# Optimization experiments

Measured on AMD Instinct MI355X. Metric: run time of the kernel, lower is better.

## Reference

```python
import jax, jax.numpy as jnp
import numpy as np

EPS = 1e-5

def _bn(t, gamma, beta):
    # training-mode BatchNorm2d: stats over (B,H,W), biased variance
    mean = jnp.mean(t, axis=(0, 2, 3), keepdims=True)
    var = jnp.var(t, axis=(0, 2, 3), keepdims=True)
    tn = (t - mean) * jax.lax.rsqrt(var + EPS)
    return tn * gamma[None, :, None, None] + beta[None, :, None, None]

def setup_inputs() -> dict:
    key = jax.random.key(0)
    ks = jax.random.split(key, 8)
    B, C, H, W = 16, 256, 64, 64
    u, k, v = 4, 16, 256
    s = 1.0 / np.sqrt(C)
    x = jax.random.normal(ks[0], (B, C, H, W), dtype=jnp.float32)
    Wq = jax.random.normal(ks[1], (k, C), dtype=jnp.float32) * s
    bq = jax.random.normal(ks[2], (k,), dtype=jnp.float32) * 0.01
    Wk = jax.random.normal(ks[3], (u * k, C), dtype=jnp.float32) * s
    bk = jax.random.normal(ks[4], (u * k,), dtype=jnp.float32) * 0.01
    Wv = jax.random.normal(ks[5], (u * v, C), dtype=jnp.float32) * s
    bv = jax.random.normal(ks[6], (u * v,), dtype=jnp.float32) * 0.01
    gamma_q = jnp.ones((k,), dtype=jnp.float32)
    beta_q = jnp.zeros((k,), dtype=jnp.float32)
    gamma_v = jnp.ones((u * v,), dtype=jnp.float32)
    beta_v = jnp.zeros((u * v,), dtype=jnp.float32)
    return {"x": x, "Wq": Wq, "bq": bq, "Wk": Wk, "bk": bk, "Wv": Wv, "bv": bv,
            "gamma_q": gamma_q, "beta_q": beta_q, "gamma_v": gamma_v, "beta_v": beta_v}

def reference(x, Wq, bq, Wk, bk, Wv, bv, gamma_q, beta_q, gamma_v, beta_v):
    B, C, H, W = x.shape
    k = Wq.shape[0]
    u = 4
    v = Wv.shape[0] // u
    # 1x1 convs as channel contractions
    Q = jnp.einsum('oc,bchw->bohw', Wq, x) + bq[None, :, None, None]   # [B,k,H,W]
    K = jnp.einsum('oc,bchw->bohw', Wk, x) + bk[None, :, None, None]   # [B,u*k,H,W]
    V = jnp.einsum('oc,bchw->bohw', Wv, x) + bv[None, :, None, None]   # [B,u*v,H,W]
    Q = _bn(Q, gamma_q, beta_q)
    V = _bn(V, gamma_v, beta_v)
    m = H * W
    Q = Q.reshape(B, k, m)          # [B,k,m]
    K = K.reshape(B, u, k, m)       # [B,u,k,m]
    V = V.reshape(B, u, v, m)       # [B,u,v,m]
    K = jax.nn.softmax(K, axis=3)
    context = jnp.einsum('bukm,buvm->bkv', K, V)   # [B,k,v]
    y = jnp.einsum('bkn,bkv->bvn', Q, context)     # [B,v,m]
    return y.reshape(B, v, H, W)
```

## Files before the change

### kernel.cpp

```cpp
#include <hip/hip_runtime.h>
#include <hip/hip_bf16.h>

typedef short s16x8 __attribute__((ext_vector_type(8)));
typedef short s16x4 __attribute__((ext_vector_type(4)));
typedef float f32x4 __attribute__((ext_vector_type(4)));
typedef unsigned u32;
typedef u32 u32x2 __attribute__((ext_vector_type(2)));

#define DI __device__ __forceinline__

constexpr int BB = 16;
constexpr int CC = 256;
constexpr int MM = 4096;
constexpr int KD = 16;
constexpr int UK = 64;
constexpr float EPSV = 1e-5f;

DI unsigned short f2bf(float f) {
  union { float f; unsigned u; } v; v.f = f;
  unsigned r = v.u + 0x7FFFu + ((v.u >> 16) & 1u);
  return (unsigned short)(r >> 16);
}
DI float bfu(unsigned short u) { union { u32 u; float f; } w; w.u = (u32)u << 16; return w.f; }
DI float bflo(u32 v) { union { u32 u; float f; } w; w.u = v << 16; return w.f; }
DI float bfhi(u32 v) { union { u32 u; float f; } w; w.u = v & 0xFFFF0000u; return w.f; }

__global__ __launch_bounds__(256) void k_cvt(const float* __restrict__ x,
    unsigned short* __restrict__ xbf, float* __restrict__ xsump) {
  int bid = blockIdx.x;
  size_t base = (size_t)bid * MM;
  int t = threadIdx.x;
  float s = 0.f;
#pragma unroll
  for (int i = 0; i < 4; ++i) {
    size_t idx = base + (size_t)(i * 256 + t) * 4;
    float4 v = *(const float4*)(x + idx);
    s16x4 c;
    c[0] = (short)f2bf(v.x); c[1] = (short)f2bf(v.y);
    c[2] = (short)f2bf(v.z); c[3] = (short)f2bf(v.w);
    *(s16x4*)&xbf[idx] = c;
    s += v.x + v.y + v.z + v.w;
  }
#pragma unroll
  for (int o = 32; o; o >>= 1) s += __shfl_down(s, o);
  __shared__ float red[4];
  if ((t & 63) == 0) red[t >> 6] = s;
  __syncthreads();
  if (t == 0) xsump[bid] = red[0] + red[1] + red[2] + red[3];
}

__global__ __launch_bounds__(512) void k_gxx(const unsigned short* __restrict__ xbf,
                                             u32* __restrict__ part) {
  int b = blockIdx.x >> 4, mc = blockIdx.x & 15;
  int m0 = mc * 256;
  __shared__ short lds[2][256 * 72];
  int t = threadIdx.x, w = t >> 6, l = t & 63;
  int wr = w >> 2, wc = w & 3;
  int lrow = l & 15, lk8 = (l >> 4) * 8;
  int srow = t >> 3, sseg = (t & 7) * 8;

  const unsigned short* gsrc = xbf + ((size_t)(b * CC + srow)) * MM + m0 + sseg;

  s16x8 rg[4];
#pragma unroll
  for (int i = 0; i < 4; ++i)
    rg[i] = *(const s16x8*)(gsrc + (size_t)i * 64 * MM);
#pragma unroll
  for (int i = 0; i < 4; ++i)
    *(s16x8*)&lds[0][(srow + i * 64) * 72 + sseg] = rg[i];

  f32x4 acc[8][4];
#pragma unroll
  for (int i = 0; i < 8; ++i)
#pragma unroll
    for (int j = 0; j < 4; ++j) acc[i][j] = (f32x4)0.f;

#pragma unroll
  for (int ks = 0; ks < 4; ++ks) {
    __syncthreads();
    if (ks < 3) {
#pragma unroll
      for (int i = 0; i < 4; ++i)
        rg[i] = *(const s16x8*)(gsrc + (size_t)i * 64 * MM + (ks + 1) * 64);
    }
    int buf = ks & 1;
#pragma unroll
    for (int half = 0; half < 2; ++half) {
      s16x8 af[8], bf[4];
#pragma unroll
      for (int i = 0; i < 8; ++i)
        af[i] = *(const s16x8*)&lds[buf][(wr * 128 + i * 16 + lrow) * 72 + half * 32 + lk8];
#pragma unroll
      for (int j = 0; j < 4; ++j)
        bf[j] = *(const s16x8*)&lds[buf][(wc * 64 + j * 16 + lrow) * 72 + half * 32 + lk8];
#pragma unroll
      for (int i = 0; i < 8; ++i)
#pragma unroll
        for (int j = 0; j < 4; ++j)
          acc[i][j] = __builtin_amdgcn_mfma_f32_16x16x32_bf16(af[i], bf[j], acc[i][j], 0, 0, 0);
    }
    if (ks < 3) {
#pragma unroll
      for (int i = 0; i < 4; ++i)
        *(s16x8*)&lds[buf ^ 1][(srow + i * 64) * 72 + sseg] = rg[i];
    }
  }

  size_t pb = (size_t)blockIdx.x * 32768;
#pragma unroll
  for (int i = 0; i < 8; ++i)
#pragma unroll
    for (int j = 0; j < 4; ++j) {
      int tau = (w * 8 + i) * 4 + j;
      u32x2 pk;
      pk[0] = (u32)f2bf(acc[i][j][0]) | ((u32)f2bf(acc[i][j][1]) << 16);
      pk[1] = (u32)f2bf(acc[i][j][2]) | ((u32)f2bf(acc[i][j][3]) << 16);
      *(u32x2*)&part[pb + tau * 128 + l * 2] = pk;
    }
}

__global__ __launch_bounds__(256) void k_gred(const u32* __restrict__ part,
                                              float* __restrict__ G) {
  int q = blockIdx.x * 256 + threadIdx.x;
  float s0 = 0.f, s1 = 0.f;
#pragma unroll 8
  for (int p = 0; p < 256; ++p) {
    u32 v = part[(size_t)p * 32768 + q];
    s0 += bflo(v);
    s1 += bfhi(v);
  }
  int r2 = q & 1, l = (q >> 1) & 63, tau = q >> 7;
  int j = tau & 3, i = (tau >> 2) & 7, w = tau >> 5;
  int wr = w >> 2, wc = w & 3;
  int row = wr * 128 + i * 16 + (l >> 4) * 4 + r2 * 2;
  int col = wc * 64 + j * 16 + (l & 15);
  G[row * 256 + col] = s0;
  G[(row + 1) * 256 + col] = s1;
}

__global__ __launch_bounds__(256) void k_proj(const unsigned short* __restrict__ xbf,
    const float* __restrict__ Wq, const float* __restrict__ bq,
    const float* __restrict__ Wk, const float* __restrict__ bk,
    unsigned short* __restrict__ Kbf, unsigned short* __restrict__ Qbf,
    float* __restrict__ pstat) {
  int b = blockIdx.x >> 5, mc = blockIdx.x & 31;
  int gm0 = mc * 128;
  __shared__ u32 xt[2][128 * 17];
  __shared__ short wb[2][80 * 40];
  __shared__ float smax[4][64], ssum[4][64];
  int t = threadIdx.x;
  int w = t >> 6, l = t & 63;
  int lrow = l & 15, lk = l >> 4;
  int c2 = t >> 4;
  int mq = t & 15;
  int wrow0 = t >> 3;
  int wcol = (t & 7) * 4;

  s16x4 xv[2][2];
  float4 wv[3];

  {
    const unsigned short* p0 = xbf + ((size_t)(b * CC + 2 * c2)) * MM + gm0 + mq * 4;
#pragma unroll
    for (int mb = 0; mb < 2; ++mb) {
      xv[mb][0] = *(const s16x4*)(p0 + mb * 64);
      xv[mb][1] = *(const s16x4*)(p0 + mb * 64 + MM);
    }
#pragma unroll
    for (int rep = 0; rep < 3; ++rep) {
      int row = rep * 32 + wrow0;
      if (row < 80)
        wv[rep] = *(const float4*)((row < 64 ? Wk + (size_t)row * CC
                                             : Wq + (size_t)(row - 64) * CC) + wcol);
    }
#pragma unroll
    for (int mb = 0; mb < 2; ++mb) {
      int m = mb * 64 + mq * 4;
#pragma unroll
      for (int i = 0; i < 4; ++i)
        xt[0][(m + i) * 17 + c2] =
            (u32)(unsigned short)xv[mb][0][i] | ((u32)(unsigned short)xv[mb][1][i] << 16);
    }
#pragma unroll
    for (int rep = 0; rep < 3; ++rep) {
      int row = rep * 32 + wrow0;
      if (row < 80) {
        s16x4 wc4;
        wc4[0] = (short)f2bf(wv[rep].x); wc4[1] = (short)f2bf(wv[rep].y);
        wc4[2] = (short)f2bf(wv[rep].z); wc4[3] = (short)f2bf(wv[rep].w);
        *(s16x4*)&wb[0][row * 40 + wcol] = wc4;
      }
    }
  }
  __syncthreads();

  f32x4 acc[5][2];
#pragma unroll
  for (int i = 0; i < 5; ++i) { acc[i][0] = (f32x4)0.f; acc[i][1] = (f32x4)0.f; }

  for (int ks = 0; ks < 8; ++ks) {
    int buf = ks & 1;
    if (ks < 7) {
      int c0 = (ks + 1) * 32;
      const unsigned short* p0 = xbf + ((size_t)(b * CC + c0 + 2 * c2)) * MM + gm0 + mq * 4;
#pragma unroll
      for (int mb = 0; mb < 2; ++mb) {
        xv[mb][0] = *(const s16x4*)(p0 + mb * 64);
        xv[mb][1] = *(const s16x4*)(p0 + mb * 64 + MM);
      }
#pragma unroll
      for (int rep = 0; rep < 3; ++rep) {
        int row = rep * 32 + wrow0;
        if (row < 80)
          wv[rep] = *(const float4*)((row < 64 ? Wk + (size_t)row * CC
                                               : Wq + (size_t)(row - 64) * CC) + c0 + wcol);
      }
    }
    union { s16x8 v; u32 wd[4]; } bfr[2];
#pragma unroll
    for (int j = 0; j < 2; ++j) {
      int ml = w * 32 + j * 16 + lrow;
#pragma unroll
      for (int i = 0; i < 4; ++i) bfr[j].wd[i] = xt[buf][ml * 17 + lk * 4 + i];
    }
#pragma unroll
    for (int ot = 0; ot < 5; ++ot) {
      s16x8 af = *(const s16x8*)&wb[buf][(ot * 16 + lrow) * 40 + lk * 8];
      acc[ot][0] = __builtin_amdgcn_mfma_f32_16x16x32_bf16(af, bfr[0].v, acc[ot][0], 0, 0, 0);
      acc[ot][1] = __builtin_amdgcn_mfma_f32_16x16x32_bf16(af, bfr[1].v, acc[ot][1], 0, 0, 0);
    }
    if (ks < 7) {
#pragma unroll
      for (int mb = 0; mb < 2; ++mb) {
        int m = mb * 64 + mq * 4;
#pragma unroll
        for (int i = 0; i < 4; ++i)
          xt[buf ^ 1][(m + i) * 17 + c2] =
              (u32)(unsigned short)xv[mb][0][i] | ((u32)(unsigned short)xv[mb][1][i] << 16);
      }
#pragma unroll
      for (int rep = 0; rep < 3; ++rep) {
        int row = rep * 32 + wrow0;
        if (row < 80) {
          s16x4 wc4;
          wc4[0] = (short)f2bf(wv[rep].x); wc4[1] = (short)f2bf(wv[rep].y);
          wc4[2] = (short)f2bf(wv[rep].z); wc4[3] = (short)f2bf(wv[rep].w);
          *(s16x4*)&wb[buf ^ 1][row * 40 + wcol] = wc4;
        }
      }
    }
    __syncthreads();
  }

  int mcol = gm0 + w * 32 + lrow;
#pragma unroll
  for (int ot = 0; ot < 4; ++ot)
#pragma unroll
    for (int r = 0; r < 4; ++r) {
      int o = ot * 16 + lk * 4 + r;
      float bias = bk[o];
      unsigned short u0 = f2bf(acc[ot][0][r] + bias);
      unsigned short u1 = f2bf(acc[ot][1][r] + bias);
      size_t rowoff = ((size_t)(b * UK + o)) * MM;
      Kbf[rowoff + mcol] = u0;
      Kbf[rowoff + mcol + 16] = u1;
      float rv0 = bfu(u0), rv1 = bfu(u1);
      float mx = fmaxf(rv0, rv1);
      mx = fmaxf(mx, __shfl_xor(mx, 1));
      mx = fmaxf(mx, __shfl_xor(mx, 2));
      mx = fmaxf(mx, __shfl_xor(mx, 4));
      mx = fmaxf(mx, __shfl_xor(mx, 8));
      float se = __expf(rv0 - mx) + __expf(rv1 - mx);
      se += __shfl_xor(se, 1);
      se += __shfl_xor(se, 2);
      se += __shfl_xor(se, 4);
      se += __shfl_xor(se, 8);
      if (lrow == 0) { smax[w][o] = mx; ssum[w][o] = se; }
    }
#pragma unroll
  for (int r = 0; r < 4; ++r) {
    int oq = lk * 4 + r;
    float bias = bq[oq];
    size_t rowoff = ((size_t)(b * KD + oq)) * MM;
    Qbf[rowoff + mcol] = f2bf(acc[4][0][r] + bias);
    Qbf[rowoff + mcol + 16] = f2bf(acc[4][1][r] + bias);
  }
  __syncthreads();
  if (t < 64) {
    float m0_ = smax[0][t], m1_ = smax[1][t], m2_ = smax[2][t], m3_ = smax[3][t];
    float mm = fmaxf(fmaxf(m0_, m1_), fmaxf(m2_, m3_));
    float ss = ssum[0][t] * __expf(m0_ - mm) + ssum[1][t] * __expf(m1_ - mm) +
               ssum[2][t] * __expf(m2_ - mm) + ssum[3][t] * __expf(m3_ - mm);
    size_t po = ((size_t)blockIdx.x * 64 + t) * 2;
    pstat[po] = mm;
    pstat[po + 1] = ss;
  }
}

__global__ __launch_bounds__(64) void k_pmerge(const float* __restrict__ pstat,
    float* __restrict__ rmax, float* __restrict__ rsum) {
  int b = blockIdx.x, o = threadIdx.x;
  float mm = -3.4e38f;
#pragma unroll 8
  for (int mc = 0; mc < 32; ++mc)
    mm = fmaxf(mm, pstat[((size_t)((b * 32 + mc) * 64 + o)) * 2]);
  float ss = 0.f;
#pragma unroll 8
  for (int mc = 0; mc < 32; ++mc) {
    size_t po = ((size_t)((b * 32 + mc) * 64 + o)) * 2;
    ss += pstat[po + 1] * __expf(pstat[po] - mm);
  }
  rmax[b * 64 + o] = mm;
  rsum[b * 64 + o] = ss;
}

__global__ __launch_bounds__(256) void k_fin(const float* __restrict__ G,
    const float* __restrict__ xsump,
    const float* __restrict__ Wv, const float* __restrict__ bv,
    const float* __restrict__ gv, const float* __restrict__ btv,
    const float* __restrict__ Wq, const float* __restrict__ bq,
    const float* __restrict__ gq, const float* __restrict__ btq,
    float* __restrict__ AV, float* __restrict__ BVa,
    float* __restrict__ AQ, float* __restrict__ BQa) {
  int t = threadIdx.x, w = t >> 6, l = t & 63;
  int o0 = blockIdx.x * 4;
  __shared__ float lw[4][256];
#pragma unroll
  for (int oo = 0; oo < 4; ++oo) {
    int o = o0 + oo;
    lw[oo][t] = (o < 1024) ? Wv[(size_t)o * CC + t] : Wq[(size_t)(o - 1024) * CC + t];
  }
  __syncthreads();

  float4 w4[4];
#pragma unroll
  for (int oo = 0; oo < 4; ++oo) w4[oo] = *(const float4*)&lw[oo][4 * l];

  float qf[4] = {0.f, 0.f, 0.f, 0.f};
#pragma unroll 4
  for (int i = 0; i < 64; ++i) {
    int r = i * 4 + w;
    float4 g4 = *(const float4*)(G + (size_t)r * CC + 4 * l);
#pragma unroll
    for (int oo = 0; oo < 4; ++oo) {
      float d = g4.x * w4[oo].x + g4.y * w4[oo].y + g4.z * w4[oo].z + g4.w * w4[oo].w;
      qf[oo] = fmaf(lw[oo][r], d, qf[oo]);
    }
  }

  float xs = 0.f;
#pragma unroll
  for (int bb = 0; bb < 16; ++bb) xs += xsump[bb * 256 + t];
  float sx[4];
#pragma unroll
  for (int oo = 0; oo < 4; ++oo) sx[oo] = lw[oo][t] * xs;

#pragma unroll
  for (int oo = 0; oo < 4; ++oo)
#pragma unroll
    for (int od = 32; od; od >>= 1) {
      qf[oo] += __shfl_xor(qf[oo], od);
      sx[oo] += __shfl_xor(sx[oo], od);
    }
  __shared__ float rq[4][4], rs[4][4];
  if (l == 0)
#pragma unroll
    for (int oo = 0; oo < 4; ++oo) { rq[w][oo] = qf[oo]; rs[w][oo] = sx[oo]; }
  __syncthreads();
  if (t < 4) {
    int oo = t, o = o0 + oo;
    float q = rq[0][oo] + rq[1][oo] + rq[2][oo] + rq[3][oo];
    float s = rs[0][oo] + rs[1][oo] + rs[2][oo] + rs[3][oo];
    float bias, gamma, beta; float *pa, *pb;
    if (o < 1024) { bias = bv[o]; gamma = gv[o]; beta = btv[o]; pa = AV + o; pb = BVa + o; }
    else { int oi = o - 1024; bias = bq[oi]; gamma = gq[oi]; beta = btq[oi]; pa = AQ + oi; pb = BQa + oi; }
    const float invN = 1.f / 65536.f;
    float mean = s * invN + bias;
    float e2 = q * invN + 2.f * bias * s * invN + bias * bias;
    float var = e2 - mean * mean;
    float a = gamma * rsqrtf(var + EPSV);
    *pa = a;
    *pb = beta - mean * a;
  }
}

__global__ __launch_bounds__(256) void k_xp(const unsigned short* __restrict__ xbf,
    const unsigned short* __restrict__ Kbf, const float* __restrict__ rmax,
    float* __restrict__ xpp) {
  int b = blockIdx.x >> 4, kc = blockIdx.x & 15;
  int kbase = kc * 256;
  __shared__ short la[64][40];
  __shared__ short lb[256][40];
  int t = threadIdx.x, w = t >> 6, l = t & 63;
  int lrow = l & 15, lk = (l >> 4) * 8;

  f32x4 acc[4][4];
#pragma unroll
  for (int i = 0; i < 4; ++i)
#pragma unroll
    for (int j = 0; j < 4; ++j) acc[i][j] = (f32x4)0.f;

  for (int ks = 0; ks < 8; ++ks) {
    int k0 = kbase + ks * 32;
    __syncthreads();
    {
      int r = t >> 2, sg = (t & 3) * 8;
      s16x8 kv = *(const s16x8*)&Kbf[((size_t)(b * UK + r)) * MM + k0 + sg];
      float rm = rmax[b * UK + r];
      s16x8 wv;
#pragma unroll
      for (int i = 0; i < 8; ++i)
        wv[i] = (short)f2bf(__expf(bfu((unsigned short)kv[i]) - rm));
      *(s16x8*)&la[r][sg] = wv;
    }
#pragma unroll
    for (int i = 0; i < 4; ++i) {
      int r = i * 64 + (t >> 2), sg = (t & 3) * 8;
      s16x8 v = *(const s16x8*)&xbf[((size_t)(b * CC + r)) * MM + k0 + sg];
      *(s16x8*)&lb[r][sg] = v;
    }
    __syncthreads();
    s16x8 af[4], bfr[4];
#pragma unroll
    for (int i = 0; i < 4; ++i) af[i] = *(const s16x8*)&la[i * 16 + lrow][lk];
#pragma unroll
    for (int j = 0; j < 4; ++j) bfr[j] = *(const s16x8*)&lb[w * 64 + j * 16 + lrow][lk];
#pragma unroll
    for (int i = 0; i < 4; ++i)
#pragma unroll
      for (int j = 0; j < 4; ++j)
        acc[i][j] = __builtin_amdgcn_mfma_f32_16x16x32_bf16(af[i], bfr[j], acc[i][j], 0, 0, 0);
  }
  float* dst = xpp + (size_t)blockIdx.x * UK * CC;
#pragma unroll
  for (int i = 0; i < 4; ++i)
#pragma unroll
    for (int j = 0; j < 4; ++j)
#pragma unroll
      for (int r = 0; r < 4; ++r) {
        int row = i * 16 + (l >> 4) * 4 + r;
        int col = w * 64 + j * 16 + lrow;
        dst[row * 256 + col] = acc[i][j][r];
      }
}

__global__ __launch_bounds__(256) void k_prep(const float* __restrict__ xpp,
    const float* __restrict__ rsum, const float* __restrict__ Wv,
    const float* __restrict__ AV, unsigned short* __restrict__ xpn,
    unsigned short* __restrict__ wvs) {
  int t = threadIdx.x;
  if (blockIdx.x < 256) {
    int b = blockIdx.x >> 4, kk = blockIdx.x & 15;
    unsigned short* dst = xpn + ((size_t)(b * 16 + kk)) * 1024;
#pragma unroll
    for (int u = 0; u < 4; ++u) {
      int row = u * 16 + kk;
      float s = 0.f;
#pragma unroll
      for (int kc = 0; kc < 16; ++kc)
        s += xpp[((size_t)(b * 16 + kc) * UK + row) * CC + t];
      s /= rsum[b * UK + row];
      dst[u * 256 + t] = f2bf(s);
    }
  } else {
    int ch = blockIdx.x - 256;
    float a = AV[ch];
    wvs[(size_t)ch * CC + t] = f2bf(a * Wv[(size_t)ch * CC + t]);
  }
}

__global__ __launch_bounds__(64) void k_ctx2(const unsigned short* __restrict__ xpn,
    const unsigned short* __restrict__ wvs,
    const float* __restrict__ AV, const float* __restrict__ bv,
    const float* __restrict__ BVa, float* __restrict__ CTX) {
  int mt = blockIdx.x >> 3, nt = blockIdx.x & 7;
  int m0 = mt * 32, n0 = nt * 32;
  int l = threadIdx.x;
  int lrow = l & 15, lk8 = (l >> 4) * 8;

  f32x4 acc[2][2];
#pragma unroll
  for (int i = 0; i < 2; ++i)
#pragma unroll
    for (int j = 0; j < 2; ++j) acc[i][j] = (f32x4)0.f;

#pragma unroll 4
  for (int k0 = 0; k0 < 1024; k0 += 32) {
    int u = k0 >> 8, c0 = k0 & 255;
    s16x8 a0 = *(const s16x8*)&xpn[(size_t)(m0 + lrow) * 1024 + k0 + lk8];
    s16x8 a1 = *(const s16x8*)&xpn[(size_t)(m0 + 16 + lrow) * 1024 + k0 + lk8];
    s16x8 b0 = *(const s16x8*)&wvs[(size_t)(u * 256 + n0 + lrow) * CC + c0 + lk8];
    s16x8 b1 = *(const s16x8*)&wvs[(size_t)(u * 256 + n0 + 16 + lrow) * CC + c0 + lk8];
    acc[0][0] = __builtin_amdgcn_mfma_f32_16x16x32_bf16(a0, b0, acc[0][0], 0, 0, 0);
    acc[0][1] = __builtin_amdgcn_mfma_f32_16x16x32_bf16(a0, b1, acc[0][1], 0, 0, 0);
    acc[1][0] = __builtin_amdgcn_mfma_f32_16x16x32_bf16(a1, b0, acc[1][0], 0, 0, 0);
    acc[1][1] = __builtin_amdgcn_mfma_f32_16x16x32_bf16(a1, b1, acc[1][1], 0, 0, 0);
  }

  float cst[2];
#pragma unroll
  for (int j = 0; j < 2; ++j) {
    int vv = n0 + j * 16 + lrow;
    float s = 0.f;
#pragma unroll
    for (int u = 0; u < 4; ++u) {
      int ch = u * 256 + vv;
      s += AV[ch] * bv[ch] + BVa[ch];
    }
    cst[j] = s;
  }

#pragma unroll
  for (int i = 0; i < 2; ++i)
#pragma unroll
    for (int j = 0; j < 2; ++j)
#pragma unroll
      for (int r = 0; r < 4; ++r) {
        int row = m0 + i * 16 + (l >> 4) * 4 + r;
        int col = n0 + j * 16 + lrow;
        CTX[(size_t)row * 256 + col] = acc[i][j][r] + cst[j];
      }
}

__global__ __launch_bounds__(256) void k_y(const unsigned short* __restrict__ Qbf,
    const float* __restrict__ CTX,
    const float* __restrict__ AQ, const float* __restrict__ BQa,
    float* __restrict__ y) {
  int b = blockIdx.x >> 4, nc = blockIdx.x & 15;
  int m = nc * 256 + threadIdx.x;
  float qn[16];
#pragma unroll
  for (int kk = 0; kk < 16; ++kk)
    qn[kk] = AQ[kk] * bfu(Qbf[((size_t)b * KD + kk) * MM + m]) + BQa[kk];
  const float* cb = CTX + (size_t)b * KD * 256;
  float* yo = y + (size_t)b * 256 * MM + m;
#pragma unroll 4
  for (int vv = 0; vv < 256; ++vv) {
    float acc = 0.f;
#pragma unroll
    for (int kk = 0; kk < 16; ++kk)
      acc = fmaf(qn[kk], cb[kk * 256 + vv], acc);
    yo[(size_t)vv * MM] = acc;
  }
}

extern "C" void kernel_launch(void* const* d_in, const int* in_sizes, int n_in,
                              void* d_out, int out_size, void* d_ws, size_t ws_size,
                              hipStream_t stream) {
  const float* x   = (const float*)d_in[0];
  const float* Wq  = (const float*)d_in[1];
  const float* bq  = (const float*)d_in[2];
  const float* Wk  = (const float*)d_in[3];
  const float* bk  = (const float*)d_in[4];
  const float* Wv  = (const float*)d_in[5];
  const float* bv  = (const float*)d_in[6];
  const float* gq  = (const float*)d_in[7];
  const float* btq = (const float*)d_in[8];
  const float* gv  = (const float*)d_in[9];
  const float* btv = (const float*)d_in[10];
  float* out = (float*)d_out;
  float* ws  = (float*)d_ws;

  float* G     = ws;
  float* XSUMP = ws + 65536;
  float* PSTAT = ws + 69632;
  float* RMAX  = ws + 135168;
  float* RSUM  = ws + 136192;
  float* AV    = ws + 137216;
  float* BVa   = ws + 138240;
  float* AQ    = ws + 139264;
  float* BQa   = ws + 139280;
  float* CTX   = ws + 139520;
  u32*  PART   = (u32*)(ws + 205056);
  float* XPP   = ws + 205056;
  unsigned short* KBf = (unsigned short*)(ws + 4399360);
  unsigned short* QBf = (unsigned short*)(ws + 6496512);
  unsigned short* XBF = (unsigned short*)(ws + 8593664);
  unsigned short* XPN = (unsigned short*)(ws + 16982272);
  unsigned short* WVS = (unsigned short*)(ws + 17113344);

  k_cvt   <<<4096, 256, 0, stream>>>(x, XBF, XSUMP);
  k_gxx   <<<256,  512, 0, stream>>>(XBF, PART);
  k_gred  <<<128,  256, 0, stream>>>(PART, G);
  k_proj  <<<512,  256, 0, stream>>>(XBF, Wq, bq, Wk, bk, KBf, QBf, PSTAT);
  k_pmerge<<<16,   64,  0, stream>>>(PSTAT, RMAX, RSUM);
  k_fin   <<<260,  256, 0, stream>>>(G, XSUMP, Wv, bv, gv, btv, Wq, bq, gq, btq,
                                     AV, BVa, AQ, BQa);
  k_xp    <<<256,  256, 0, stream>>>(XBF, KBf, RMAX, XPP);
  k_prep  <<<1280, 256, 0, stream>>>(XPP, RSUM, Wv, AV, XPN, WVS);
  k_ctx2  <<<64,   64,  0, stream>>>(XPN, WVS, AV, bv, BVa, CTX);
  k_y     <<<256,  256, 0, stream>>>(QBf, CTX, AQ, BQa, out);
}
```

Before: 145.5 us.

## Halve k_proj tile width and double-buffer k_xp shared-memory loads

```diff
diff --git a/kernel.cpp b/kernel.cpp
--- a/kernel.cpp
+++ b/kernel.cpp
@@ -143,9 +143,9 @@
     const float* __restrict__ Wk, const float* __restrict__ bk,
     unsigned short* __restrict__ Kbf, unsigned short* __restrict__ Qbf,
     float* __restrict__ pstat) {
-  int b = blockIdx.x >> 5, mc = blockIdx.x & 31;
-  int gm0 = mc * 128;
-  __shared__ u32 xt[2][128 * 17];
+  int b = blockIdx.x >> 6, mc = blockIdx.x & 63;
+  int gm0 = mc * 64;
+  __shared__ u32 xt[2][64 * 17];
   __shared__ short wb[2][80 * 40];
   __shared__ float smax[4][64], ssum[4][64];
   int t = threadIdx.x;
@@ -156,16 +156,13 @@
   int wrow0 = t >> 3;
   int wcol = (t & 7) * 4;
 
-  s16x4 xv[2][2];
+  s16x4 xv0, xv1;
   float4 wv[3];
 
   {
     const unsigned short* p0 = xbf + ((size_t)(b * CC + 2 * c2)) * MM + gm0 + mq * 4;
-#pragma unroll
-    for (int mb = 0; mb < 2; ++mb) {
-      xv[mb][0] = *(const s16x4*)(p0 + mb * 64);
-      xv[mb][1] = *(const s16x4*)(p0 + mb * 64 + MM);
-    }
+    xv0 = *(const s16x4*)p0;
+    xv1 = *(const s16x4*)(p0 + MM);
 #pragma unroll
     for (int rep = 0; rep < 3; ++rep) {
       int row = rep * 32 + wrow0;
@@ -174,13 +171,9 @@
                                              : Wq + (size_t)(row - 64) * CC) + wcol);
     }
 #pragma unroll
-    for (int mb = 0; mb < 2; ++mb) {
-      int m = mb * 64 + mq * 4;
-#pragma unroll
-      for (int i = 0; i < 4; ++i)
-        xt[0][(m + i) * 17 + c2] =
-            (u32)(unsigned short)xv[mb][0][i] | ((u32)(unsigned short)xv[mb][1][i] << 16);
-    }
+    for (int i = 0; i < 4; ++i)
+      xt[0][(mq * 4 + i) * 17 + c2] =
+          (u32)(unsigned short)xv0[i] | ((u32)(unsigned short)xv1[i] << 16);
 #pragma unroll
     for (int rep = 0; rep < 3; ++rep) {
       int row = rep * 32 + wrow0;
@@ -194,20 +187,17 @@
   }
   __syncthreads();
 
-  f32x4 acc[5][2];
-#pragma unroll
-  for (int i = 0; i < 5; ++i) { acc[i][0] = (f32x4)0.f; acc[i][1] = (f32x4)0.f; }
+  f32x4 acc[5];
+#pragma unroll
+  for (int i = 0; i < 5; ++i) acc[i] = (f32x4)0.f;
 
   for (int ks = 0; ks < 8; ++ks) {
     int buf = ks & 1;
     if (ks < 7) {
       int c0 = (ks + 1) * 32;
       const unsigned short* p0 = xbf + ((size_t)(b * CC + c0 + 2 * c2)) * MM + gm0 + mq * 4;
-#pragma unroll
-      for (int mb = 0; mb < 2; ++mb) {
-        xv[mb][0] = *(const s16x4*)(p0 + mb * 64);
-        xv[mb][1] = *(const s16x4*)(p0 + mb * 64 + MM);
-      }
+      xv0 = *(const s16x4*)p0;
+      xv1 = *(const s16x4*)(p0 + MM);
 #pragma unroll
       for (int rep = 0; rep < 3; ++rep) {
         int row = rep * 32 + wrow0;
@@ -216,28 +206,20 @@
                                                : Wq + (size_t)(row - 64) * CC) + c0 + wcol);
       }
     }
-    union { s16x8 v; u32 wd[4]; } bfr[2];
-#pragma unroll
-    for (int j = 0; j < 2; ++j) {
-      int ml = w * 32 + j * 16 + lrow;
-#pragma unroll
-      for (int i = 0; i < 4; ++i) bfr[j].wd[i] = xt[buf][ml * 17 + lk * 4 + i];
-    }
+    union { s16x8 v; u32 wd[4]; } bfr;
+    int ml = w * 16 + lrow;
+#pragma unroll
+    for (int i = 0; i < 4; ++i) bfr.wd[i] = xt[buf][ml * 17 + lk * 4 + i];
 #pragma unroll
     for (int ot = 0; ot < 5; ++ot) {
       s16x8 af = *(const s16x8*)&wb[buf][(ot * 16 + lrow) * 40 + lk * 8];
-      acc[ot][0] = __builtin_amdgcn_mfma_f32_16x16x32_bf16(af, bfr[0].v, acc[ot][0], 0, 0, 0);
-      acc[ot][1] = __builtin_amdgcn_mfma_f32_16x16x32_bf16(af, bfr[1].v, acc[ot][1], 0, 0, 0);
+      acc[ot] = __builtin_amdgcn_mfma_f32_16x16x32_bf16(af, bfr.v, acc[ot], 0, 0, 0);
     }
     if (ks < 7) {
 #pragma unroll
-      for (int mb = 0; mb < 2; ++mb) {
-        int m = mb * 64 + mq * 4;
-#pragma unroll
-        for (int i = 0; i < 4; ++i)
-          xt[buf ^ 1][(m + i) * 17 + c2] =
-              (u32)(unsigned short)xv[mb][0][i] | ((u32)(unsigned short)xv[mb][1][i] << 16);
-      }
+      for (int i = 0; i < 4; ++i)
+        xt[buf ^ 1][(mq * 4 + i) * 17 + c2] =
+            (u32)(unsigned short)xv0[i] | ((u32)(unsigned short)xv1[i] << 16);
 #pragma unroll
       for (int rep = 0; rep < 3; ++rep) {
         int row = rep * 32 + wrow0;
@@ -252,25 +234,22 @@
     __syncthreads();
   }
 
-  int mcol = gm0 + w * 32 + lrow;
+  int mcol = gm0 + w * 16 + lrow;
 #pragma unroll
   for (int ot = 0; ot < 4; ++ot)
 #pragma unroll
     for (int r = 0; r < 4; ++r) {
       int o = ot * 16 + lk * 4 + r;
       float bias = bk[o];
-      unsigned short u0 = f2bf(acc[ot][0][r] + bias);
-      unsigned short u1 = f2bf(acc[ot][1][r] + bias);
-      size_t rowoff = ((size_t)(b * UK + o)) * MM;
-      Kbf[rowoff + mcol] = u0;
-      Kbf[rowoff + mcol + 16] = u1;
-      float rv0 = bfu(u0), rv1 = bfu(u1);
-      float mx = fmaxf(rv0, rv1);
+      unsigned short u0 = f2bf(acc[ot][r] + bias);
+      Kbf[((size_t)(b * UK + o)) * MM + mcol] = u0;
+      float rv0 = bfu(u0);
+      float mx = rv0;
       mx = fmaxf(mx, __shfl_xor(mx, 1));
       mx = fmaxf(mx, __shfl_xor(mx, 2));
       mx = fmaxf(mx, __shfl_xor(mx, 4));
       mx = fmaxf(mx, __shfl_xor(mx, 8));
-      float se = __expf(rv0 - mx) + __expf(rv1 - mx);
+      float se = __expf(rv0 - mx);
       se += __shfl_xor(se, 1);
       se += __shfl_xor(se, 2);
       se += __shfl_xor(se, 4);
@@ -280,10 +259,7 @@
 #pragma unroll
   for (int r = 0; r < 4; ++r) {
     int oq = lk * 4 + r;
-    float bias = bq[oq];
-    size_t rowoff = ((size_t)(b * KD + oq)) * MM;
-    Qbf[rowoff + mcol] = f2bf(acc[4][0][r] + bias);
-    Qbf[rowoff + mcol + 16] = f2bf(acc[4][1][r] + bias);
+    Qbf[((size_t)(b * KD + oq)) * MM + mcol] = f2bf(acc[4][r] + bq[oq]);
   }
   __syncthreads();
   if (t < 64) {
@@ -302,12 +278,12 @@
   int b = blockIdx.x, o = threadIdx.x;
   float mm = -3.4e38f;
 #pragma unroll 8
-  for (int mc = 0; mc < 32; ++mc)
-    mm = fmaxf(mm, pstat[((size_t)((b * 32 + mc) * 64 + o)) * 2]);
+  for (int mc = 0; mc < 64; ++mc)
+    mm = fmaxf(mm, pstat[((size_t)((b * 64 + mc) * 64 + o)) * 2]);
   float ss = 0.f;
 #pragma unroll 8
-  for (int mc = 0; mc < 32; ++mc) {
-    size_t po = ((size_t)((b * 32 + mc) * 64 + o)) * 2;
+  for (int mc = 0; mc < 64; ++mc) {
+    size_t po = ((size_t)((b * 64 + mc) * 64 + o)) * 2;
     ss += pstat[po + 1] * __expf(pstat[po] - mm);
   }
   rmax[b * 64 + o] = mm;
@@ -389,10 +365,33 @@
     float* __restrict__ xpp) {
   int b = blockIdx.x >> 4, kc = blockIdx.x & 15;
   int kbase = kc * 256;
-  __shared__ short la[64][40];
-  __shared__ short lb[256][40];
+  __shared__ short la[2][64 * 40];
+  __shared__ short lb[2][256 * 40];
   int t = threadIdx.x, w = t >> 6, l = t & 63;
   int lrow = l & 15, lk = (l >> 4) * 8;
+  int ra = t >> 2, sga = (t & 3) * 8;
+
+  float rm = rmax[b * UK + ra];
+  const unsigned short* ksrc = Kbf + ((size_t)(b * UK + ra)) * MM + kbase + sga;
+  const unsigned short* xsrc = xbf + ((size_t)(b * CC + ra)) * MM + kbase + sga;
+
+  s16x8 kv, xv[4];
+
+  kv = *(const s16x8*)ksrc;
+#pragma unroll
+  for (int i = 0; i < 4; ++i)
+    xv[i] = *(const s16x8*)(xsrc + (size_t)i * 64 * MM);
+  {
+    s16x8 ev;
+#pragma unroll
+    for (int i = 0; i < 8; ++i)
+      ev[i] = (short)f2bf(__expf(bfu((unsigned short)kv[i]) - rm));
+    *(s16x8*)&la[0][ra * 40 + sga] = ev;
+#pragma unroll
+    for (int i = 0; i < 4; ++i)
+      *(s16x8*)&lb[0][(ra + i * 64) * 40 + sga] = xv[i];
+  }
+  __syncthreads();
 
   f32x4 acc[4][4];
 #pragma unroll
@@ -401,36 +400,37 @@
     for (int j = 0; j < 4; ++j) acc[i][j] = (f32x4)0.f;
 
   for (int ks = 0; ks < 8; ++ks) {
-    int k0 = kbase + ks * 32;
-    __syncthreads();
-    {
-      int r = t >> 2, sg = (t & 3) * 8;
-      s16x8 kv = *(const s16x8*)&Kbf[((size_t)(b * UK + r)) * MM + k0 + sg];
-      float rm = rmax[b * UK + r];
-      s16x8 wv;
-#pragma unroll
-      for (int i = 0; i < 8; ++i)
-        wv[i] = (short)f2bf(__expf(bfu((unsigned short)kv[i]) - rm));
-      *(s16x8*)&la[r][sg] = wv;
-    }
-#pragma unroll
-    for (int i = 0; i < 4; ++i) {
-      int r = i * 64 + (t >> 2), sg = (t & 3) * 8;
-      s16x8 v = *(const s16x8*)&xbf[((size_t)(b * CC + r)) * MM + k0 + sg];
-      *(s16x8*)&lb[r][sg] = v;
-    }
-    __syncthreads();
+    int buf = ks & 1;
+    if (ks < 7) {
+      int k1 = (ks + 1) * 32;
+      kv = *(const s16x8*)(ksrc + k1);
+#pragma unroll
+      for (int i = 0; i < 4; ++i)
+        xv[i] = *(const s16x8*)(xsrc + (size_t)i * 64 * MM + k1);
+    }
     s16x8 af[4], bfr[4];
 #pragma unroll
-    for (int i = 0; i < 4; ++i) af[i] = *(const s16x8*)&la[i * 16 + lrow][lk];
-#pragma unroll
-    for (int j = 0; j < 4; ++j) bfr[j] = *(const s16x8*)&lb[w * 64 + j * 16 + lrow][lk];
+    for (int i = 0; i < 4; ++i) af[i] = *(const s16x8*)&la[buf][(i * 16 + lrow) * 40 + lk];
+#pragma unroll
+    for (int j = 0; j < 4; ++j) bfr[j] = *(const s16x8*)&lb[buf][(w * 64 + j * 16 + lrow) * 40 + lk];
 #pragma unroll
     for (int i = 0; i < 4; ++i)
 #pragma unroll
       for (int j = 0; j < 4; ++j)
         acc[i][j] = __builtin_amdgcn_mfma_f32_16x16x32_bf16(af[i], bfr[j], acc[i][j], 0, 0, 0);
-  }
+    if (ks < 7) {
+      s16x8 ev;
+#pragma unroll
+      for (int i = 0; i < 8; ++i)
+        ev[i] = (short)f2bf(__expf(bfu((unsigned short)kv[i]) - rm));
+      *(s16x8*)&la[buf ^ 1][ra * 40 + sga] = ev;
+#pragma unroll
+      for (int i = 0; i < 4; ++i)
+        *(s16x8*)&lb[buf ^ 1][(ra + i * 64) * 40 + sga] = xv[i];
+    }
+    __syncthreads();
+  }
+
   float* dst = xpp + (size_t)blockIdx.x * UK * CC;
 #pragma unroll
   for (int i = 0; i < 4; ++i)
@@ -564,25 +564,25 @@
   float* G     = ws;
   float* XSUMP = ws + 65536;
   float* PSTAT = ws + 69632;
-  float* RMAX  = ws + 135168;
-  float* RSUM  = ws + 136192;
-  float* AV    = ws + 137216;
-  float* BVa   = ws + 138240;
-  float* AQ    = ws + 139264;
-  float* BQa   = ws + 139280;
-  float* CTX   = ws + 139520;
-  u32*  PART   = (u32*)(ws + 205056);
-  float* XPP   = ws + 205056;
-  unsigned short* KBf = (unsigned short*)(ws + 4399360);
-  unsigned short* QBf = (unsigned short*)(ws + 6496512);
-  unsigned short* XBF = (unsigned short*)(ws + 8593664);
-  unsigned short* XPN = (unsigned short*)(ws + 16982272);
-  unsigned short* WVS = (unsigned short*)(ws + 17113344);
+  float* RMAX  = ws + 200704;
+  float* RSUM  = ws + 201728;
+  float* AV    = ws + 202752;
+  float* BVa   = ws + 203776;
+  float* AQ    = ws + 204800;
+  float* BQa   = ws + 204816;
+  float* CTX   = ws + 205056;
+  u32*  PART   = (u32*)(ws + 270592);
+  float* XPP   = ws + 270592;
+  unsigned short* KBf = (unsigned short*)(ws + 4464896);
+  unsigned short* QBf = (unsigned short*)(ws + 6562048);
+  unsigned short* XBF = (unsigned short*)(ws + 8659200);
+  unsigned short* XPN = (unsigned short*)(ws + 17047808);
+  unsigned short* WVS = (unsigned short*)(ws + 17178880);
 
   k_cvt   <<<4096, 256, 0, stream>>>(x, XBF, XSUMP);
   k_gxx   <<<256,  512, 0, stream>>>(XBF, PART);
   k_gred  <<<128,  256, 0, stream>>>(PART, G);
-  k_proj  <<<512,  256, 0, stream>>>(XBF, Wq, bq, Wk, bk, KBf, QBf, PSTAT);
+  k_proj  <<<1024, 256, 0, stream>>>(XBF, Wq, bq, Wk, bk, KBf, QBf, PSTAT);
   k_pmerge<<<16,   64,  0, stream>>>(PSTAT, RMAX, RSUM);
   k_fin   <<<260,  256, 0, stream>>>(G, XSUMP, Wv, bv, gv, btv, Wq, bq, gq, btq,
                                      AV, BVa, AQ, BQa);
```

Result: slower. 150.3 us (+3.3%).
